# Kernel tuning notes

Measured on AMD Instinct MI355X. Metric: run time of the kernel, lower is better.

The kernel has to match this reference:

```python
import jax, jax.numpy as jnp
import numpy as np
from functools import partial

SOM_SHAPE = (100, 100)
INPUT_SIZE = 256
BATCH = 1024
INIT_LR = 0.5
INIT_RADIUS = max(SOM_SHAPE) / 2.0  # 50.0


def setup_inputs() -> dict:
    key = jax.random.key(0)
    k1, k2 = jax.random.split(key)
    x = jax.random.normal(k1, (BATCH, INPUT_SIZE), dtype=jnp.float32)
    weights = jax.random.normal(k2, (*SOM_SHAPE, INPUT_SIZE), dtype=jnp.float32) * 0.1
    return {"x": x, "weights": weights, "epoch": 10, "total_epochs": 100}


def reference(x, weights, epoch, total_epochs):
    H, W = SOM_SHAPE
    decay = 1.0 - epoch / total_epochs
    lr = jnp.float32(INIT_LR * decay)
    radius = jnp.float32(INIT_RADIUS * decay)

    # --- get_bmu: squared euclidean distances x (B,D) vs weights (H*W,D) ---
    wf = weights.reshape(-1, INPUT_SIZE)                       # (HW, D)
    d2 = (jnp.sum(x * x, axis=1, keepdims=True)                # (B, 1)
          - 2.0 * (x @ wf.T)                                   # (B, HW)
          + jnp.sum(wf * wf, axis=1))                          # (HW,)
    bmu_idx = jnp.argmin(d2, axis=1)                           # (B,)
    by = (bmu_idx // W).astype(jnp.float32)                    # (B,)
    bx = (bmu_idx % W).astype(jnp.float32)

    # --- get_neighborhood: gaussian over grid distance to BMU ---
    yy = jnp.arange(H, dtype=jnp.float32)[:, None]             # (H, 1)
    xx = jnp.arange(W, dtype=jnp.float32)[None, :]             # (1, W)
    grid_d2 = ((by[:, None, None] - yy) ** 2
               + (bx[:, None, None] - xx) ** 2)                # (B, H, W)
    neigh = jnp.exp(-grid_d2 / (2.0 * radius ** 2))            # (B, H, W)

    # --- update_weights: sequential per-sample EMA update (recurrence) ---
    def step(w, inp):
        xi, ni = inp  # (D,), (H, W)
        w = w + lr * ni[..., None] * (xi[None, None, :] - w)
        return w, None

    new_weights, _ = jax.lax.scan(step, weights, (x, neigh))
    return new_weights
```

## Files before the change

kernel.cpp:

```cpp
#include <hip/hip_runtime.h>
#include <hip/hip_fp16.h>

typedef unsigned long long ull;
typedef unsigned short ushort_t;
typedef unsigned int u32;
typedef short bf16x8 __attribute__((ext_vector_type(8)));
typedef _Float16 f16x8 __attribute__((ext_vector_type(8)));
typedef float f32x4 __attribute__((ext_vector_type(4)));

#define NC 10000
#define D_ 256
#define B_ 1024
#define W_ 100
#define NTC 157
#define LD 10240
#define FIXMARGIN 0.06f
#define SHORTCAP 128

__device__ __forceinline__ void gl_lds16(const void* g, void* l) {
    __builtin_amdgcn_global_load_lds(
        (const __attribute__((address_space(1))) u32*)g,
        (__attribute__((address_space(3))) u32*)l,
        16, 0, 0);
}

__device__ __forceinline__ int xcd_swz(int orig, int nwg) {
    int q = nwg >> 3, r = nwg & 7;
    int xcd = orig & 7, off = orig >> 3;
    return (xcd < r ? xcd * (q + 1) : r * (q + 1) + (xcd - r) * q) + off;
}

__device__ __forceinline__ unsigned fkey(float f) {
    unsigned u = __float_as_uint(f);
    return (u & 0x80000000u) ? ~u : (u | 0x80000000u);
}
__device__ __forceinline__ float unfkey(unsigned k) {
    unsigned u = (k & 0x80000000u) ? (k ^ 0x80000000u) : ~k;
    return __uint_as_float(u);
}

__device__ __forceinline__ ushort_t f2bf(float f) {
    unsigned u = __float_as_uint(f);
    unsigned r = (u + 0x7fffu + ((u >> 16) & 1u)) >> 16;
    return (ushort_t)r;
}

__device__ __forceinline__ void decay_params(const int* ep, const int* tp, float& lr, float& inv2r2) {
    double decay = 1.0 - (double)(*ep) / (double)(*tp);
    lr = (float)(0.5 * decay);
    float radius = (float)(50.0 * decay);
    inv2r2 = 1.0f / (2.0f * radius * radius);
}

__global__ __launch_bounds__(256) void k_prep(const float* __restrict__ w, const float* __restrict__ x,
                                              __half* __restrict__ wh, float* __restrict__ wnorm,
                                              __half* __restrict__ xh, ushort_t* __restrict__ xhT,
                                              ull* __restrict__ pk1) {
    int bid = blockIdx.x;
    int tid = threadIdx.x;
    if (bid < NC / 4) {
        int cell = bid * 4 + (tid >> 6);
        int lane = tid & 63;
        float4 v = *reinterpret_cast<const float4*>(&w[(size_t)cell * D_ + lane * 4]);
        float s = v.x * v.x + v.y * v.y + v.z * v.z + v.w * v.w;
        __half hb[4];
        float e[4] = {v.x, v.y, v.z, v.w};
        #pragma unroll
        for (int i = 0; i < 4; ++i) hb[i] = __float2half(e[i]);
        *reinterpret_cast<uint2*>(&wh[(size_t)cell * D_ + lane * 4]) = *reinterpret_cast<uint2*>(hb);
        #pragma unroll
        for (int off = 32; off; off >>= 1) s += __shfl_xor(s, off);
        if (lane == 0) wnorm[cell] = s;
    } else if (bid < NC / 4 + 64) {
        __shared__ ushort_t tile[64][65];
        int idx = bid - NC / 4;
        int b0 = (idx & 15) * 64, d0 = (idx >> 4) * 64;
        #pragma unroll
        for (int r = 0; r < 16; ++r) {
            int f = r * 256 + tid;
            int i = f >> 6, j = f & 63;
            float v = x[(size_t)(b0 + i) * D_ + d0 + j];
            xh[(size_t)(b0 + i) * D_ + d0 + j] = __float2half(v);
            tile[j][i] = f2bf(v);
        }
        __syncthreads();
        #pragma unroll
        for (int r = 0; r < 2; ++r) {
            int f = r * 256 + tid;
            int row = f >> 3, u = f & 7;
            ushort_t v[8];
            #pragma unroll
            for (int e = 0; e < 8; ++e) v[e] = tile[row][u * 8 + e];
            *reinterpret_cast<uint4*>(&xhT[(size_t)(d0 + row) * B_ + b0 + u * 8]) =
                *reinterpret_cast<uint4*>(v);
        }
    } else {
        #pragma unroll
        for (int k = 0; k < 4; ++k) pk1[tid * 4 + k] = ~0ull;
        if (tid < 128) wnorm[NC + tid] = __builtin_inff();
    }
}

__global__ __launch_bounds__(512) void k_scores_mfma(const __half* __restrict__ wh, const __half* __restrict__ xh,
                                                     const float* __restrict__ wnorm, __half* __restrict__ h,
                                                     ull* __restrict__ pk1) {
    __shared__ __align__(16) __half As[64 * 64];
    __shared__ __align__(16) __half Bs[128 * 64];
    const int tid = threadIdx.x;
    int orig = blockIdx.y * gridDim.x + blockIdx.x;
    int wgid = xcd_swz(orig, 8 * NTC);
    const int b0 = (wgid & 7) * 128;
    const int c0 = (wgid >> 3) * 64;
    const int wid = tid >> 6, lane = tid & 63;
    const int wc = wid >> 2;
    const int wb = wid & 3;
    const int g4 = lane >> 4, l16 = lane & 15;

    f32x4 acc[2][2] = {};

    for (int k0 = 0; k0 < D_; k0 += 64) {
        if (k0) __syncthreads();
        {
            int row = tid >> 3, u = tid & 7;
            int ug = (u ^ (row & 7)) * 8;
            int cc = c0 + row; if (cc > NC - 1) cc = NC - 1;
            gl_lds16(&wh[(size_t)cc * D_ + k0 + ug], &As[(tid & ~63) * 8]);
        }
        #pragma unroll
        for (int r = 0; r < 2; ++r) {
            int f = tid + r * 512;
            int row = f >> 3, u = f & 7;
            int ug = (u ^ (row & 7)) * 8;
            gl_lds16(&xh[(size_t)(b0 + row) * D_ + k0 + ug], &Bs[(f & ~63) * 8]);
        }
        __syncthreads();
        #pragma unroll
        for (int kh = 0; kh < 2; ++kh) {
            int ubase = kh * 4 + g4;
            f16x8 bfr[2];
            #pragma unroll
            for (int fn = 0; fn < 2; ++fn) {
                int rowb = wb * 32 + fn * 16 + l16;
                bfr[fn] = *reinterpret_cast<const f16x8*>(&Bs[rowb * 64 + ((ubase ^ (rowb & 7)) * 8)]);
            }
            #pragma unroll
            for (int fm = 0; fm < 2; ++fm) {
                int rowa = wc * 32 + fm * 16 + l16;
                f16x8 af = *reinterpret_cast<const f16x8*>(&As[rowa * 64 + ((ubase ^ (rowa & 7)) * 8)]);
                #pragma unroll
                for (int fn = 0; fn < 2; ++fn)
                    acc[fm][fn] = __builtin_amdgcn_mfma_f32_16x16x32_f16(af, bfr[fn], acc[fm][fn], 0, 0, 0);
            }
        }
    }

    #pragma unroll
    for (int fm = 0; fm < 2; ++fm) {
        int cb = c0 + wc * 32 + fm * 16 + g4 * 4;
        #pragma unroll
        for (int fn = 0; fn < 2; ++fn) {
            int b = b0 + wb * 32 + fn * 16 + l16;
            __half hv[4];
            #pragma unroll
            for (int r = 0; r < 4; ++r) hv[r] = __float2half(acc[fm][fn][r]);
            *reinterpret_cast<uint2*>(&h[(size_t)b * LD + cb]) = *reinterpret_cast<uint2*>(hv);
        }
    }

    ull best[2] = {~0ull, ~0ull};
    #pragma unroll
    for (int fm = 0; fm < 2; ++fm) {
        int cb = c0 + wc * 32 + fm * 16 + g4 * 4;
        float4 wn4 = *reinterpret_cast<const float4*>(&wnorm[cb]);
        float wna[4] = {wn4.x, wn4.y, wn4.z, wn4.w};
        #pragma unroll
        for (int fn = 0; fn < 2; ++fn)
            #pragma unroll
            for (int r = 0; r < 4; ++r) {
                float s = wna[r] - 2.0f * acc[fm][fn][r];
                ull p = ((ull)fkey(s) << 32) | (unsigned)(cb + r);
                if (p < best[fn]) best[fn] = p;
            }
    }
    #pragma unroll
    for (int fn = 0; fn < 2; ++fn) {
        ull o = __shfl_xor(best[fn], 16); best[fn] = o < best[fn] ? o : best[fn];
        o = __shfl_xor(best[fn], 32);     best[fn] = o < best[fn] ? o : best[fn];
    }
    if (g4 == 0) {
        atomicMin(&pk1[b0 + wb * 32 + l16], best[0]);
        atomicMin(&pk1[b0 + wb * 32 + 16 + l16], best[1]);
    }
}

__global__ __launch_bounds__(256) void k_fix(const __half* __restrict__ h, const float* __restrict__ wnorm,
                                             const float* __restrict__ x, const float* __restrict__ w,
                                             const ull* __restrict__ pk1, int2* __restrict__ bxy) {
    __shared__ int cnt;
    __shared__ int cand[SHORTCAP];
    __shared__ ull sbest[4];
    int b = blockIdx.x, tid = threadIdx.x;
    if (tid == 0) cnt = 0;
    __syncthreads();
    float thr = unfkey((unsigned)(pk1[b] >> 32)) + FIXMARGIN;
    for (int ch = 0; ch < 10; ++ch) {
        int c = ch * 1024 + tid * 4;
        if (c < NC) {
            __half hv[4];
            *reinterpret_cast<uint2*>(hv) = *reinterpret_cast<const uint2*>(&h[(size_t)b * LD + c]);
            float4 wn = *reinterpret_cast<const float4*>(&wnorm[c]);
            float we[4] = {wn.x, wn.y, wn.z, wn.w};
            #pragma unroll
            for (int e = 0; e < 4; ++e) {
                float s = we[e] - 2.0f * (float)hv[e];
                if (s <= thr) {
                    int p = atomicAdd(&cnt, 1);
                    if (p < SHORTCAP) cand[p] = c + e;
                }
            }
        }
    }
    __syncthreads();
    int n = cnt;
    int wid = tid >> 6, lane = tid & 63;
    float4 xv = *reinterpret_cast<const float4*>(&x[(size_t)b * D_ + lane * 4]);
    ull best = ~0ull;
    if (n <= SHORTCAP) {
        for (int i = wid; i < n; i += 4) {
            int c = cand[i];
            float4 wv = *reinterpret_cast<const float4*>(&w[(size_t)c * D_ + lane * 4]);
            float p = wv.x * (wv.x - 2.0f * xv.x) + wv.y * (wv.y - 2.0f * xv.y)
                    + wv.z * (wv.z - 2.0f * xv.z) + wv.w * (wv.w - 2.0f * xv.w);
            #pragma unroll
            for (int off = 32; off; off >>= 1) p += __shfl_xor(p, off);
            if (lane == 0) {
                ull pk = ((ull)fkey(p) << 32) | (unsigned)c;
                best = pk < best ? pk : best;
            }
        }
    } else {
        for (int c = wid; c < NC; c += 4) {
            float4 wv = *reinterpret_cast<const float4*>(&w[(size_t)c * D_ + lane * 4]);
            float p = wv.x * (wv.x - 2.0f * xv.x) + wv.y * (wv.y - 2.0f * xv.y)
                    + wv.z * (wv.z - 2.0f * xv.z) + wv.w * (wv.w - 2.0f * xv.w);
            #pragma unroll
            for (int off = 32; off; off >>= 1) p += __shfl_xor(p, off);
            if (lane == 0) {
                ull pk = ((ull)fkey(p) << 32) | (unsigned)c;
                best = pk < best ? pk : best;
            }
        }
    }
    if (lane == 0) sbest[wid] = best;
    __syncthreads();
    if (tid == 0) {
        ull bb = sbest[0];
        #pragma unroll
        for (int k = 1; k < 4; ++k) bb = sbest[k] < bb ? sbest[k] : bb;
        int c = (int)(unsigned)(bb & 0xffffffffull);
        bxy[b] = make_int2(c / W_, c % W_);
    }
}

__global__ __launch_bounds__(256) void k_scan(const int2* __restrict__ bxy, const int* __restrict__ ep,
                                              const int* __restrict__ tp, ushort_t* __restrict__ coefT,
                                              float* __restrict__ T) {
    __shared__ float E[W_];
    float lr, inv2r2;
    decay_params(ep, tp, lr, inv2r2);
    if (threadIdx.x < W_) {
        float d = (float)threadIdx.x;
        E[threadIdx.x] = __expf(-d * d * inv2r2);
    }
    __syncthreads();

    int g = blockIdx.x * 256 + threadIdx.x;
    int c = g >> 3, t = g & 7;
    if (c >= NC) return;
    int cy = c / W_, cx = c % W_;
    int base = t * 128;

    float P = 1.0f;
    for (int i = base; i < base + 128; ++i) {
        int2 p = bxy[i];
        int dy = abs(p.x - cy), dx = abs(p.y - cx);
        float a = lr * E[dy] * E[dx];
        P *= (1.0f - a);
    }
    int gbase = (threadIdx.x & 63) & ~7;
    float M = 1.0f;
    #pragma unroll
    for (int k = 1; k < 8; ++k) {
        float pk = __shfl(P, gbase + k, 64);
        if (k > t) M *= pk;
    }
    if (t == 0) T[c] = M * P;

    float s = M;
    for (int seg = 15; seg >= 0; --seg) {
        ushort_t buf[8];
        #pragma unroll
        for (int e = 7; e >= 0; --e) {
            int i = base + seg * 8 + e;
            int2 p = bxy[i];
            int dy = abs(p.x - cy), dx = abs(p.y - cx);
            float a = lr * E[dy] * E[dx];
            buf[e] = f2bf(a * s);
            s *= (1.0f - a);
        }
        *reinterpret_cast<uint4*>(&coefT[(size_t)c * B_ + base + seg * 8]) =
            *reinterpret_cast<uint4*>(buf);
    }
}

__global__ __launch_bounds__(256) void k_update(const ushort_t* __restrict__ coefT, const ushort_t* __restrict__ xhT,
                                                const float* __restrict__ T, const float* __restrict__ w0,
                                                float* __restrict__ out) {
    __shared__ __align__(16) ushort_t As[32 * 64];
    __shared__ __align__(16) ushort_t Bs[64 * 64];
    const int tid = threadIdx.x;
    int orig = blockIdx.y * gridDim.x + blockIdx.x;
    int wgid = xcd_swz(orig, 4 * 313);
    const int d0 = (wgid & 3) * 64;
    const int c0 = (wgid >> 2) * 32;
    const int wid = tid >> 6, lane = tid & 63;
    const int wc = wid >> 1, wd = wid & 1;
    const int g4 = lane >> 4, l16 = lane & 15;

    f32x4 acc[2] = {};

    for (int k0 = 0; k0 < B_; k0 += 64) {
        if (k0) __syncthreads();
        {
            int row = tid >> 3, u = tid & 7;
            int ug = (u ^ (row & 7)) * 8;
            int cc = c0 + row; if (cc > NC - 1) cc = NC - 1;
            gl_lds16(&coefT[(size_t)cc * B_ + k0 + ug], &As[(tid & ~63) * 8]);
        }
        #pragma unroll
        for (int r = 0; r < 2; ++r) {
            int f = tid + r * 256;
            int row = f >> 3, u = f & 7;
            int ug = (u ^ (row & 7)) * 8;
            gl_lds16(&xhT[(size_t)(d0 + row) * B_ + k0 + ug], &Bs[(f & ~63) * 8]);
        }
        __syncthreads();
        #pragma unroll
        for (int kh = 0; kh < 2; ++kh) {
            int ubase = kh * 4 + g4;
            int rowa = wc * 16 + l16;
            bf16x8 af = *reinterpret_cast<const bf16x8*>(&As[rowa * 64 + ((ubase ^ (rowa & 7)) * 8)]);
            #pragma unroll
            for (int fn = 0; fn < 2; ++fn) {
                int rowb = wd * 32 + fn * 16 + l16;
                bf16x8 bfr = *reinterpret_cast<const bf16x8*>(&Bs[rowb * 64 + ((ubase ^ (rowb & 7)) * 8)]);
                acc[fn] = __builtin_amdgcn_mfma_f32_16x16x32_bf16(af, bfr, acc[fn], 0, 0, 0);
            }
        }
    }

    #pragma unroll
    for (int r = 0; r < 4; ++r) {
        int c = c0 + wc * 16 + g4 * 4 + r;
        if (c < NC) {
            float t = T[c];
            #pragma unroll
            for (int fn = 0; fn < 2; ++fn) {
                int d = d0 + wd * 32 + fn * 16 + l16;
                out[(size_t)c * D_ + d] = fmaf(t, w0[(size_t)c * D_ + d], acc[fn][r]);
            }
        }
    }
}

__global__ void k_initfix(ull* packed_fix) {
    int i = blockIdx.x * 256 + threadIdx.x;
    if (i < B_) packed_fix[i] = ~0ull;
}
__global__ __launch_bounds__(256) void k_exact_bmu(const float* __restrict__ x, const float* __restrict__ w,
                                                   ull* __restrict__ packed_fix) {
    int b = blockIdx.x;
    int wid = threadIdx.x >> 6, lane = threadIdx.x & 63;
    float4 xv = *reinterpret_cast<const float4*>(&x[(size_t)b * D_ + lane * 4]);
    ull best = ~0ull;
    for (int c = wid; c < NC; c += 4) {
        float4 wv = *reinterpret_cast<const float4*>(&w[(size_t)c * D_ + lane * 4]);
        float p = wv.x * (wv.x - 2.0f * xv.x) + wv.y * (wv.y - 2.0f * xv.y)
                + wv.z * (wv.z - 2.0f * xv.z) + wv.w * (wv.w - 2.0f * xv.w);
        #pragma unroll
        for (int off = 32; off; off >>= 1) p += __shfl_xor(p, off);
        if (lane == 0) {
            ull pk = ((ull)fkey(p) << 32) | (unsigned)c;
            best = pk < best ? pk : best;
        }
    }
    if (lane == 0) atomicMin(&packed_fix[b], best);
}
__global__ void k_decode_force(const ull* __restrict__ packed_fix, float2* __restrict__ xy) {
    int i = blockIdx.x * 256 + threadIdx.x;
    if (i < B_) {
        int c = (int)(unsigned)(packed_fix[i] & 0xffffffffull);
        xy[i] = make_float2((float)(c / W_), (float)(c % W_));
    }
}
__global__ __launch_bounds__(256) void k_update_fallback(const float* __restrict__ x, const float* __restrict__ w0,
                                                         const float2* __restrict__ xy, const int* ep, const int* tp,
                                                         float* __restrict__ out) {
    int c = blockIdx.x;
    int d = threadIdx.x;
    float cyf = (float)(c / W_), cxf = (float)(c % W_);
    float lr, inv2r2;
    decay_params(ep, tp, lr, inv2r2);
    float acc = w0[(size_t)c * D_ + d];
    for (int i = 0; i < B_; ++i) {
        float2 p = xy[i];
        float dy = p.x - cyf, dx = p.y - cxf;
        float a = lr * __expf(-(dy * dy + dx * dx) * inv2r2);
        acc = fmaf(a, x[(size_t)i * D_ + d] - acc, acc);
    }
    out[(size_t)c * D_ + d] = acc;
}

extern "C" void kernel_launch(void* const* d_in, const int* in_sizes, int n_in,
                              void* d_out, int out_size, void* d_ws, size_t ws_size,
                              hipStream_t stream) {
    const float* x = (const float*)d_in[0];
    const float* w = (const float*)d_in[1];
    const int* ep = (const int*)d_in[2];
    const int* tp = (const int*)d_in[3];
    float* out = (float*)d_out;

    char* ws = (char*)d_ws;
    ull* pk1        = (ull*)ws;
    int2* bxy       = (int2*)(ws + 16384);
    float2* xyf     = (float2*)(ws + 16384);
    float* T        = (float*)(ws + 24576);
    float* wnorm    = (float*)(ws + 65536);
    ushort_t* xhT   = (ushort_t*)(ws + 131072);
    __half* xh      = (__half*)(ws + 655360);
    __half* wh      = (__half*)(ws + 1179648);
    ushort_t* coefT = (ushort_t*)(ws + 6553600);
    __half* h       = (__half*)(ws + 27262976);
    size_t required = 27262976 + (size_t)B_ * LD * 2;

    if (ws_size >= required) {
        k_prep<<<NC / 4 + 64 + 1, 256, 0, stream>>>(w, x, wh, wnorm, xh, xhT, pk1);
        k_scores_mfma<<<dim3(8, NTC), 512, 0, stream>>>(wh, xh, wnorm, h, pk1);
        k_fix<<<B_, 256, 0, stream>>>(h, wnorm, x, w, pk1, bxy);
        k_scan<<<(NC * 8 + 255) / 256, 256, 0, stream>>>(bxy, ep, tp, coefT, T);
        k_update<<<dim3(4, 313), 256, 0, stream>>>(coefT, xhT, T, w, out);
    } else {
        k_initfix<<<4, 256, 0, stream>>>(pk1);
        k_exact_bmu<<<B_, 256, 0, stream>>>(x, w, pk1);
        k_decode_force<<<4, 256, 0, stream>>>(pk1, xyf);
        k_update_fallback<<<NC, 256, 0, stream>>>(x, w, xyf, ep, tp, out);
    }
}
```

Baseline: 85.32 us.

## Fuse coefficient scan into update GEMM, keeping coefficients in LDS

Merges the scan kernel that builds the per-cell bf16 coefficient matrix into the update GEMM. Each 512-thread block computes coefficients for its 32 cells directly into shared memory, splitting the batch over 16 threads per cell. The block then runs the MFMA update over all 256 feature columns. This removes the 20MB global write and re-read of coefT, plus one launch. In exchange it uses only 313 blocks with large LDS (96KB), which lowers occupancy, and the scan work sits on the GEMM's critical path with no overlap.

```diff
diff --git a/kernel.cpp b/kernel.cpp
--- a/kernel.cpp
+++ b/kernel.cpp
@@ -262,98 +262,90 @@
     }
 }
 
-__global__ __launch_bounds__(256) void k_scan(const int2* __restrict__ bxy, const int* __restrict__ ep,
-                                              const int* __restrict__ tp, ushort_t* __restrict__ coefT,
-                                              float* __restrict__ T) {
-    __shared__ float E[W_];
+__global__ __launch_bounds__(512) void k_supd(const int2* __restrict__ bxy, const int* __restrict__ ep,
+                                              const int* __restrict__ tp, const ushort_t* __restrict__ xhT,
+                                              const float* __restrict__ w0, float* __restrict__ out) {
+    extern __shared__ __align__(16) char smem[];
+    ushort_t* coefL = (ushort_t*)smem;
+    ushort_t* Bs    = (ushort_t*)(smem + 65536);
+    float* E        = (float*)(smem + 65536);
+    float* Tl       = (float*)(smem + 65536 + 512);
+
+    const int tid = threadIdx.x;
+    const int c0 = blockIdx.x * 32;
+    const int wid = tid >> 6, lane = tid & 63;
+    const int wc = wid >> 2;
+    const int wd = wid & 3;
+    const int g4 = lane >> 4, l16 = lane & 15;
+
     float lr, inv2r2;
     decay_params(ep, tp, lr, inv2r2);
-    if (threadIdx.x < W_) {
-        float d = (float)threadIdx.x;
-        E[threadIdx.x] = __expf(-d * d * inv2r2);
-    }
-    __syncthreads();
-
-    int g = blockIdx.x * 256 + threadIdx.x;
-    int c = g >> 3, t = g & 7;
-    if (c >= NC) return;
-    int cy = c / W_, cx = c % W_;
-    int base = t * 128;
-
-    float P = 1.0f;
-    for (int i = base; i < base + 128; ++i) {
-        int2 p = bxy[i];
-        int dy = abs(p.x - cy), dx = abs(p.y - cx);
-        float a = lr * E[dy] * E[dx];
-        P *= (1.0f - a);
-    }
-    int gbase = (threadIdx.x & 63) & ~7;
-    float M = 1.0f;
-    #pragma unroll
-    for (int k = 1; k < 8; ++k) {
-        float pk = __shfl(P, gbase + k, 64);
-        if (k > t) M *= pk;
-    }
-    if (t == 0) T[c] = M * P;
-
-    float s = M;
-    for (int seg = 15; seg >= 0; --seg) {
-        ushort_t buf[8];
-        #pragma unroll
-        for (int e = 7; e >= 0; --e) {
-            int i = base + seg * 8 + e;
+    if (tid < W_) E[tid] = __expf(-(float)tid * (float)tid * inv2r2);
+    __syncthreads();
+    {
+        int cl = tid >> 4;
+        int t = tid & 15;
+        int c = c0 + cl; if (c > NC - 1) c = NC - 1;
+        int cy = c / W_, cx = c % W_;
+        int base = t * 64;
+        float P = 1.0f;
+        for (int i = base; i < base + 64; ++i) {
             int2 p = bxy[i];
             int dy = abs(p.x - cy), dx = abs(p.y - cx);
-            float a = lr * E[dy] * E[dx];
-            buf[e] = f2bf(a * s);
-            s *= (1.0f - a);
-        }
-        *reinterpret_cast<uint4*>(&coefT[(size_t)c * B_ + base + seg * 8]) =
-            *reinterpret_cast<uint4*>(buf);
-    }
-}
-
-__global__ __launch_bounds__(256) void k_update(const ushort_t* __restrict__ coefT, const ushort_t* __restrict__ xhT,
-                                                const float* __restrict__ T, const float* __restrict__ w0,
-                                                float* __restrict__ out) {
-    __shared__ __align__(16) ushort_t As[32 * 64];
-    __shared__ __align__(16) ushort_t Bs[64 * 64];
-    const int tid = threadIdx.x;
-    int orig = blockIdx.y * gridDim.x + blockIdx.x;
-    int wgid = xcd_swz(orig, 4 * 313);
-    const int d0 = (wgid & 3) * 64;
-    const int c0 = (wgid >> 2) * 32;
-    const int wid = tid >> 6, lane = tid & 63;
-    const int wc = wid >> 1, wd = wid & 1;
-    const int g4 = lane >> 4, l16 = lane & 15;
-
-    f32x4 acc[2] = {};
-
+            P *= (1.0f - lr * E[dy] * E[dx]);
+        }
+        int gbase = lane & ~15;
+        float M = 1.0f;
+        #pragma unroll
+        for (int k = 1; k < 16; ++k) {
+            float pk = __shfl(P, gbase + k, 64);
+            if (k > t) M *= pk;
+        }
+        if (t == 0) Tl[cl] = M * P;
+        float s = M;
+        for (int seg = 7; seg >= 0; --seg) {
+            ushort_t buf[8];
+            #pragma unroll
+            for (int e = 7; e >= 0; --e) {
+                int i = base + seg * 8 + e;
+                int2 p = bxy[i];
+                int dy = abs(p.x - cy), dx = abs(p.y - cx);
+                float a = lr * E[dy] * E[dx];
+                buf[e] = f2bf(a * s);
+                s *= (1.0f - a);
+            }
+            int uu = (t * 8 + seg) ^ (cl & 7);
+            *reinterpret_cast<uint4*>(&coefL[(cl * 128 + uu) * 8]) = *reinterpret_cast<uint4*>(buf);
+        }
+    }
+    __syncthreads();
+
+    float treg[4];
+    #pragma unroll
+    for (int r = 0; r < 4; ++r) treg[r] = Tl[wc * 16 + g4 * 4 + r];
+    __syncthreads();
+
+    f32x4 acc[4] = {};
     for (int k0 = 0; k0 < B_; k0 += 64) {
         if (k0) __syncthreads();
-        {
-            int row = tid >> 3, u = tid & 7;
-            int ug = (u ^ (row & 7)) * 8;
-            int cc = c0 + row; if (cc > NC - 1) cc = NC - 1;
-            gl_lds16(&coefT[(size_t)cc * B_ + k0 + ug], &As[(tid & ~63) * 8]);
-        }
-        #pragma unroll
-        for (int r = 0; r < 2; ++r) {
-            int f = tid + r * 256;
+        #pragma unroll
+        for (int r = 0; r < 4; ++r) {
+            int f = tid + r * 512;
             int row = f >> 3, u = f & 7;
             int ug = (u ^ (row & 7)) * 8;
-            gl_lds16(&xhT[(size_t)(d0 + row) * B_ + k0 + ug], &Bs[(f & ~63) * 8]);
+            gl_lds16(&xhT[(size_t)row * B_ + k0 + ug], &Bs[(f & ~63) * 8]);
         }
         __syncthreads();
         #pragma unroll
         for (int kh = 0; kh < 2; ++kh) {
-            int ubase = kh * 4 + g4;
             int rowa = wc * 16 + l16;
-            bf16x8 af = *reinterpret_cast<const bf16x8*>(&As[rowa * 64 + ((ubase ^ (rowa & 7)) * 8)]);
-            #pragma unroll
-            for (int fn = 0; fn < 2; ++fn) {
-                int rowb = wd * 32 + fn * 16 + l16;
-                bf16x8 bfr = *reinterpret_cast<const bf16x8*>(&Bs[rowb * 64 + ((ubase ^ (rowb & 7)) * 8)]);
+            int uu = (k0 >> 3) + ((kh * 4 + g4) ^ (rowa & 7));
+            bf16x8 af = *reinterpret_cast<const bf16x8*>(&coefL[(rowa * 128 + uu) * 8]);
+            int ub = kh * 4 + g4;
+            #pragma unroll
+            for (int fn = 0; fn < 4; ++fn) {
+                int rowb = wd * 64 + fn * 16 + l16;
+                bf16x8 bfr = *reinterpret_cast<const bf16x8*>(&Bs[rowb * 64 + ((ub ^ (rowb & 7)) * 8)]);
                 acc[fn] = __builtin_amdgcn_mfma_f32_16x16x32_bf16(af, bfr, acc[fn], 0, 0, 0);
             }
         }
@@ -363,10 +355,10 @@
     for (int r = 0; r < 4; ++r) {
         int c = c0 + wc * 16 + g4 * 4 + r;
         if (c < NC) {
-            float t = T[c];
-            #pragma unroll
-            for (int fn = 0; fn < 2; ++fn) {
-                int d = d0 + wd * 32 + fn * 16 + l16;
+            float t = treg[r];
+            #pragma unroll
+            for (int fn = 0; fn < 4; ++fn) {
+                int d = wd * 64 + fn * 16 + l16;
                 out[(size_t)c * D_ + d] = fmaf(t, w0[(size_t)c * D_ + d], acc[fn][r]);
             }
         }
@@ -434,12 +426,10 @@
     ull* pk1        = (ull*)ws;
     int2* bxy       = (int2*)(ws + 16384);
     float2* xyf     = (float2*)(ws + 16384);
-    float* T        = (float*)(ws + 24576);
     float* wnorm    = (float*)(ws + 65536);
     ushort_t* xhT   = (ushort_t*)(ws + 131072);
     __half* xh      = (__half*)(ws + 655360);
     __half* wh      = (__half*)(ws + 1179648);
-    ushort_t* coefT = (ushort_t*)(ws + 6553600);
     __half* h       = (__half*)(ws + 27262976);
     size_t required = 27262976 + (size_t)B_ * LD * 2;
 
@@ -447,8 +437,7 @@
         k_prep<<<NC / 4 + 64 + 1, 256, 0, stream>>>(w, x, wh, wnorm, xh, xhT, pk1);
         k_scores_mfma<<<dim3(8, NTC), 512, 0, stream>>>(wh, xh, wnorm, h, pk1);
         k_fix<<<B_, 256, 0, stream>>>(h, wnorm, x, w, pk1, bxy);
-        k_scan<<<(NC * 8 + 255) / 256, 256, 0, stream>>>(bxy, ep, tp, coefT, T);
-        k_update<<<dim3(4, 313), 256, 0, stream>>>(coefT, xhT, T, w, out);
+        k_supd<<<313, 512, 98304, stream>>>(bxy, ep, tp, xhT, w, out);
     } else {
         k_initfix<<<4, 256, 0, stream>>>(pk1);
         k_exact_bmu<<<B_, 256, 0, stream>>>(x, w, pk1);
```

Result: slower. 90.80 us (+6.4%).
